# Performance work log

Measured on AMD Instinct MI355X. Metric: run time of the kernel, lower is better.

Reference implementation:

```python
import jax, jax.numpy as jnp
import numpy as np

EPS = 1e-8
VOX_WIDTH = 1.0
CURV_THRESH = 0.5


def _build_kernels():
    """Nine 3x3x3 central finite-difference stencils, pre-divided by vox_width / vox_width^2."""
    def zk():
        return np.zeros((3, 3, 3), np.float32)
    ks = {}
    # first derivatives (central difference), denominator vox_width
    for name, ax in (('ddx', 0), ('ddy', 1), ('ddz', 2)):
        k = zk(); i = [1, 1, 1]
        i[ax] = 0; k[tuple(i)] = -0.5
        i[ax] = 2; k[tuple(i)] = 0.5
        ks[name] = k / VOX_WIDTH
    # pure second derivatives, denominator vox_width^2
    for name, ax in (('d2dx2', 0), ('d2dy2', 1), ('d2dz2', 2)):
        k = zk(); i = [1, 1, 1]
        i[ax] = 0; k[tuple(i)] = 1.0
        i[ax] = 1; k[tuple(i)] = -2.0
        i[ax] = 2; k[tuple(i)] = 1.0
        ks[name] = k / VOX_WIDTH ** 2
    # mixed second derivatives, denominator vox_width^2
    for name, (a, b) in (('d2dxdy', (0, 1)), ('d2dxdz', (0, 2)), ('d2dydz', (1, 2))):
        k = zk()
        for sa, sb, v in ((0, 0, 0.25), (0, 2, -0.25), (2, 0, -0.25), (2, 2, 0.25)):
            i = [1, 1, 1]; i[a] = sa; i[b] = sb; k[tuple(i)] = v
        ks[name] = k / VOX_WIDTH ** 2
    order = ['ddx', 'ddy', 'ddz', 'd2dx2', 'd2dy2', 'd2dz2', 'd2dxdy', 'd2dxdz', 'd2dydz']
    return np.stack([ks[n] for n in order])[:, None]  # [9, 1, 3, 3, 3]


_KERNELS = jnp.asarray(_build_kernels())


def setup_inputs() -> dict:
    key = jax.random.key(0)
    phi = jax.random.normal(key, (2, 1, 192, 192, 192), dtype=jnp.float32)
    return {"phi": phi}


def reference(phi):
    # all nine stencils as one valid 3D conv: [N, 9, D-2, H-2, W-2]
    g = jax.lax.conv_general_dilated(
        phi, _KERNELS, window_strides=(1, 1, 1), padding='VALID',
        dimension_numbers=('NCDHW', 'OIDHW', 'NCDHW'))
    gx, gy, gz, hxx, hyy, hzz, hxy, hxz, hyz = (g[:, i:i + 1] for i in range(9))

    mag = jnp.sqrt(gx * gx + gy * gy + gz * gz + EPS)
    mag3 = mag ** 3

    # mean curvature: sum_{i!=j} g_i^2 H_jj - 2 sum_{i<j} g_i g_j H_ij, over |grad|^3
    cross = gx * gy * hxy + gx * gz * hxz + gy * gz * hyz
    mean_c = (gx * gx * (hyy + hzz) + gy * gy * (hxx + hzz) + gz * gz * (hxx + hyy)
              - 2.0 * cross) / (mag3 + EPS)

    # gaussian curvature: laplacian/|grad| - (g^T H g)/|grad|^3
    lap = (hxx + hyy + hzz) / (mag + EPS)
    quad = (gx * gx * hxx + gy * gy * hyy + gz * gz * hzz + 2.0 * cross) / (mag3 + EPS)
    gauss = lap - quad

    k1 = mean_c + jnp.sqrt(jnp.abs(mean_c ** 2 - gauss) + EPS)
    pen = jax.nn.relu((k1 / (CURV_THRESH + EPS)) ** 2 - 1.0)

    # zero crossings of phi over 3x3x3 neighborhoods (valid -> matches conv output shape)
    mn = jax.lax.reduce_window(phi, jnp.inf, jax.lax.min, (1, 1, 3, 3, 3), (1, 1, 1, 1, 1), 'VALID')
    mx = jax.lax.reduce_window(phi, -jnp.inf, jax.lax.max, (1, 1, 3, 3, 3), (1, 1, 1, 1, 1), 'VALID')
    phi_zero = jax.lax.stop_gradient((mn * mx < 0).astype(phi.dtype))

    return jnp.sum(phi_zero * pen) / (jnp.sum(phi_zero) + EPS)
```

## Files before the change

### kernel.cpp

```cpp
#include <hip/hip_runtime.h>


typedef float v2f __attribute__((ext_vector_type(2)));

constexpr int DIM  = 192;
constexpr int ODIM = 190;
constexpr int TX = 32, TY = 32, CZ = 10;
constexpr int NTX = 6, NTY = 6, NTZ = 19;
constexpr int PLANE = DIM * DIM;
constexpr int NBLOCKS = 2 * NTZ * NTY * NTX;

struct Slice {
    v2f   q[3][4];
    float mn[6], mx[6];
};

__global__ __launch_bounds__(256) void curv_main(const float* __restrict__ phi,
                                                 double* __restrict__ acc,
                                                 int use_partials) {
    int bx = blockIdx.x;
    const int tx = bx % NTX; bx /= NTX;
    const int ty = bx % NTY; bx /= NTY;
    const int tz = bx % NTZ; bx /= NTZ;
    const int n  = bx;

    const int xbase = tx * TX, ybase = ty * TY, zbase = tz * CZ;
    const int tid = threadIdx.x;
    const int row = tid >> 3;
    const int x0  = (tid & 7) * 4;
    const float* pn = phi + (long long)n * DIM * PLANE;

    const int c4 = xbase + x0;
    int c2t = c4 + 4; if (c2t > DIM - 2) c2t = DIM - 2;
    const int c2 = c2t;
    int yoff[3];
#pragma unroll
    for (int dy = 0; dy < 3; ++dy) {
        int iy = ybase + row + dy; if (iy > DIM - 1) iy = DIM - 1;
        yoff[dy] = iy * DIM;
    }

    float4 t4[3]; float2 t2[3];
    auto pref = [&](int g) {
        int gz = zbase + g; if (gz > DIM - 1) gz = DIM - 1;
        const float* base = pn + gz * PLANE;
#pragma unroll
        for (int dy = 0; dy < 3; ++dy) {
            t4[dy] = *(const float4*)(base + yoff[dy] + c4);
            t2[dy] = *(const float2*)(base + yoff[dy] + c2);
        }
    };

    auto unpack = [&](Slice& s) {
#pragma unroll
        for (int dy = 0; dy < 3; ++dy) {
            const float4 a = t4[dy]; const float2 b = t2[dy];
            s.q[dy][0] = (v2f){a.x, a.z};
            s.q[dy][1] = (v2f){a.y, a.w};
            s.q[dy][2] = (v2f){a.z, b.x};
            s.q[dy][3] = (v2f){a.w, b.y};
            if (dy == 0) {
                s.mn[0] = a.x; s.mn[1] = a.y; s.mn[2] = a.z;
                s.mn[3] = a.w; s.mn[4] = b.x; s.mn[5] = b.y;
                s.mx[0] = a.x; s.mx[1] = a.y; s.mx[2] = a.z;
                s.mx[3] = a.w; s.mx[4] = b.x; s.mx[5] = b.y;
            } else {
                s.mn[0] = fminf(s.mn[0], a.x); s.mx[0] = fmaxf(s.mx[0], a.x);
                s.mn[1] = fminf(s.mn[1], a.y); s.mx[1] = fmaxf(s.mx[1], a.y);
                s.mn[2] = fminf(s.mn[2], a.z); s.mx[2] = fmaxf(s.mx[2], a.z);
                s.mn[3] = fminf(s.mn[3], a.w); s.mx[3] = fmaxf(s.mx[3], a.w);
                s.mn[4] = fminf(s.mn[4], b.x); s.mx[4] = fmaxf(s.mx[4], b.x);
                s.mn[5] = fminf(s.mn[5], b.y); s.mx[5] = fmaxf(s.mx[5], b.y);
            }
        }
    };

    double sp = 0.0, sc = 0.0;
    const float EPSF = 1e-8f;
    const int oy = ybase + row;

    bool vmask[4];
#pragma unroll
    for (int j = 0; j < 4; ++j)
        vmask[j] = (oy < ODIM) && (xbase + x0 + j < ODIM);

    auto compute = [&](const Slice& s0, const Slice& s1, const Slice& s2) {
        float colmn[6], colmx[6];
#pragma unroll
        for (int c = 0; c < 6; ++c) {
            colmn[c] = fminf(fminf(s0.mn[c], s1.mn[c]), s2.mn[c]);
            colmx[c] = fmaxf(fmaxf(s0.mx[c], s1.mx[c]), s2.mx[c]);
        }

        float fsp = 0.0f, fsc = 0.0f;
#pragma unroll
        for (int p = 0; p < 2; ++p) {
            v2f gx = 0.5f * (s2.q[1][p + 1] - s0.q[1][p + 1]);
            v2f gy = 0.5f * (s1.q[2][p + 1] - s1.q[0][p + 1]);
            v2f gz = 0.5f * (s1.q[1][p + 2] - s1.q[1][p]);

            v2f c2v = 2.0f * s1.q[1][p + 1];
            v2f hxx = s0.q[1][p + 1] - c2v + s2.q[1][p + 1];
            v2f hyy = s1.q[0][p + 1] - c2v + s1.q[2][p + 1];
            v2f hzz = s1.q[1][p] - c2v + s1.q[1][p + 2];

            v2f hxy = 0.25f * (s0.q[0][p + 1] - s0.q[2][p + 1]
                             - s2.q[0][p + 1] + s2.q[2][p + 1]);
            v2f hxz = 0.25f * (s0.q[1][p] - s0.q[1][p + 2]
                             - s2.q[1][p] + s2.q[1][p + 2]);
            v2f hyz = 0.25f * (s1.q[0][p] - s1.q[0][p + 2]
                             - s1.q[2][p] + s1.q[2][p + 2]);

            v2f gx2 = gx * gx, gy2 = gy * gy, gz2 = gz * gz;
            v2f mag2 = gx2 + gy2 + gz2 + EPSF;

            v2f inv1 = (v2f){ __builtin_amdgcn_rsqf(mag2.x),
                              __builtin_amdgcn_rsqf(mag2.y) };
            v2f inv3 = inv1 * inv1 * inv1;

            v2f cross = gx * gy * hxy + gx * gz * hxz + gy * gz * hyz;

            v2f mean_c = (gx2 * (hyy + hzz) + gy2 * (hxx + hzz) +
                          gz2 * (hxx + hyy) - 2.0f * cross) * inv3;
            v2f lap   = (hxx + hyy + hzz) * inv1;
            v2f quad  = (gx2 * hxx + gy2 * hyy + gz2 * hzz + 2.0f * cross) * inv3;
            v2f gauss = lap - quad;

            v2f disc = mean_c * mean_c - gauss;
            v2f sq = (v2f){ sqrtf(fabsf(disc.x) + EPSF),
                            sqrtf(fabsf(disc.y) + EPSF) };
            v2f k1 = mean_c + sq;
            v2f t  = 2.0f * k1;
            v2f pen2 = t * t - 1.0f;

#pragma unroll
            for (int e = 0; e < 2; ++e) {
                const int j = p + 2 * e;
                float pen = fmaxf(e ? pen2.y : pen2.x, 0.0f);
                float mn = fminf(fminf(colmn[j], colmn[j + 1]), colmn[j + 2]);
                float mx = fmaxf(fmaxf(colmx[j], colmx[j + 1]), colmx[j + 2]);
                if (vmask[j] && (mn * mx < 0.0f)) {
                    fsp += pen;
                    fsc += 1.0f;
                }
            }
        }
        sp += (double)fsp;
        sc += (double)fsc;
    };

    Slice s0, s1, s2;

    pref(0); unpack(s0);
    pref(1); unpack(s1);
    pref(2);

    unpack(s2); pref(3);  compute(s0, s1, s2);
    unpack(s0); pref(4);  compute(s1, s2, s0);
    unpack(s1); pref(5);  compute(s2, s0, s1);
    unpack(s2); pref(6);  compute(s0, s1, s2);
    unpack(s0); pref(7);  compute(s1, s2, s0);
    unpack(s1); pref(8);  compute(s2, s0, s1);
    unpack(s2); pref(9);  compute(s0, s1, s2);
    unpack(s0); pref(10); compute(s1, s2, s0);
    unpack(s1); pref(11); compute(s2, s0, s1);
    unpack(s2);           compute(s0, s1, s2);

#pragma unroll
    for (int off = 32; off > 0; off >>= 1) {
        sp += __shfl_down(sp, off, 64);
        sc += __shfl_down(sc, off, 64);
    }

    __shared__ double lsp[4], lsc[4];
    const int wave = tid >> 6, lane = tid & 63;
    if (lane == 0) { lsp[wave] = sp; lsc[wave] = sc; }
    __syncthreads();
    if (tid == 0) {
        double tp = lsp[0] + lsp[1] + lsp[2] + lsp[3];
        double tc = lsc[0] + lsc[1] + lsc[2] + lsc[3];
        if (use_partials) {
            acc[2 * blockIdx.x]     = tp;
            acc[2 * blockIdx.x + 1] = tc;
        } else {
            atomicAdd(&acc[0], tp);
            atomicAdd(&acc[1], tc);
        }
    }
}

__global__ __launch_bounds__(256) void curv_reduce(const double* __restrict__ part,
                                                   int nblocks, int use_partials,
                                                   float* __restrict__ out) {
    double sp = 0.0, sc = 0.0;
    if (use_partials) {
        for (int i = threadIdx.x; i < nblocks; i += 256) {
            sp += part[2 * i];
            sc += part[2 * i + 1];
        }
    } else if (threadIdx.x == 0) {
        sp = part[0]; sc = part[1];
    }
#pragma unroll
    for (int off = 32; off > 0; off >>= 1) {
        sp += __shfl_down(sp, off, 64);
        sc += __shfl_down(sc, off, 64);
    }
    __shared__ double lsp[4], lsc[4];
    const int wave = threadIdx.x >> 6, lane = threadIdx.x & 63;
    if (lane == 0) { lsp[wave] = sp; lsc[wave] = sc; }
    __syncthreads();
    if (threadIdx.x == 0) {
        double tp = lsp[0] + lsp[1] + lsp[2] + lsp[3];
        double tc = lsc[0] + lsc[1] + lsc[2] + lsc[3];
        out[0] = (float)(tp / (tc + 1e-8));
    }
}

extern "C" void kernel_launch(void* const* d_in, const int* in_sizes, int n_in,
                              void* d_out, int out_size, void* d_ws, size_t ws_size,
                              hipStream_t stream) {
    const float* phi = (const float*)d_in[0];
    float* out = (float*)d_out;
    double* acc = (double*)d_ws;

    const int use_partials = (ws_size >= (size_t)(2 * NBLOCKS) * sizeof(double)) ? 1 : 0;
    if (!use_partials) {
        hipMemsetAsync(d_ws, 0, 2 * sizeof(double), stream);
    }

    curv_main<<<NBLOCKS, 256, 0, stream>>>(phi, acc, use_partials);
    curv_reduce<<<1, 256, 0, stream>>>(acc, NBLOCKS, use_partials, out);
}
```

Before: 109.2 us.

## Deepen z-chunk, precompute x-window min/max per slice, fold stencil scale factors

Doubles the z-chunk each block walks (19 planes instead of 10), halving the number of blocks and the halo planes reloaded per block. Per-slice min/max is now reduced across the 3-wide x window during unpack, so compute does fewer min/max operations. The 0.5 and 0.25 stencil scales are folded into the curvature formulas algebraically, with EPS scaled to match, and accumulation stays in float across the chunk instead of converting to double every step. Launch bounds now request occupancy 3, and the z clamp is dropped because the new chunking never reads past the last plane.

```diff
diff --git a/kernel.cpp b/kernel.cpp
--- a/kernel.cpp
+++ b/kernel.cpp
@@ -5,19 +5,19 @@
 
 constexpr int DIM  = 192;
 constexpr int ODIM = 190;
-constexpr int TX = 32, TY = 32, CZ = 10;
-constexpr int NTX = 6, NTY = 6, NTZ = 19;
+constexpr int TX = 32, TY = 32, CZ = 19;
+constexpr int NTX = 6, NTY = 6, NTZ = 10;
 constexpr int PLANE = DIM * DIM;
 constexpr int NBLOCKS = 2 * NTZ * NTY * NTX;
 
 struct Slice {
     v2f   q[3][4];
-    float mn[6], mx[6];
+    float xmn[4], xmx[4];
 };
 
-__global__ __launch_bounds__(256) void curv_main(const float* __restrict__ phi,
-                                                 double* __restrict__ acc,
-                                                 int use_partials) {
+__global__ __launch_bounds__(256, 3) void curv_main(const float* __restrict__ phi,
+                                                    double* __restrict__ acc,
+                                                    int use_partials) {
     int bx = blockIdx.x;
     const int tx = bx % NTX; bx /= NTX;
     const int ty = bx % NTY; bx /= NTY;
@@ -42,8 +42,7 @@
 
     float4 t4[3]; float2 t2[3];
     auto pref = [&](int g) {
-        int gz = zbase + g; if (gz > DIM - 1) gz = DIM - 1;
-        const float* base = pn + gz * PLANE;
+        const float* base = pn + (zbase + g) * PLANE;
 #pragma unroll
         for (int dy = 0; dy < 3; ++dy) {
             t4[dy] = *(const float4*)(base + yoff[dy] + c4);
@@ -52,6 +51,7 @@
     };
 
     auto unpack = [&](Slice& s) {
+        float mn6[6], mx6[6];
 #pragma unroll
         for (int dy = 0; dy < 3; ++dy) {
             const float4 a = t4[dy]; const float2 b = t2[dy];
@@ -60,23 +60,29 @@
             s.q[dy][2] = (v2f){a.z, b.x};
             s.q[dy][3] = (v2f){a.w, b.y};
             if (dy == 0) {
-                s.mn[0] = a.x; s.mn[1] = a.y; s.mn[2] = a.z;
-                s.mn[3] = a.w; s.mn[4] = b.x; s.mn[5] = b.y;
-                s.mx[0] = a.x; s.mx[1] = a.y; s.mx[2] = a.z;
-                s.mx[3] = a.w; s.mx[4] = b.x; s.mx[5] = b.y;
+                mn6[0] = a.x; mn6[1] = a.y; mn6[2] = a.z;
+                mn6[3] = a.w; mn6[4] = b.x; mn6[5] = b.y;
+                mx6[0] = a.x; mx6[1] = a.y; mx6[2] = a.z;
+                mx6[3] = a.w; mx6[4] = b.x; mx6[5] = b.y;
             } else {
-                s.mn[0] = fminf(s.mn[0], a.x); s.mx[0] = fmaxf(s.mx[0], a.x);
-                s.mn[1] = fminf(s.mn[1], a.y); s.mx[1] = fmaxf(s.mx[1], a.y);
-                s.mn[2] = fminf(s.mn[2], a.z); s.mx[2] = fmaxf(s.mx[2], a.z);
-                s.mn[3] = fminf(s.mn[3], a.w); s.mx[3] = fmaxf(s.mx[3], a.w);
-                s.mn[4] = fminf(s.mn[4], b.x); s.mx[4] = fmaxf(s.mx[4], b.x);
-                s.mn[5] = fminf(s.mn[5], b.y); s.mx[5] = fmaxf(s.mx[5], b.y);
+                mn6[0] = fminf(mn6[0], a.x); mx6[0] = fmaxf(mx6[0], a.x);
+                mn6[1] = fminf(mn6[1], a.y); mx6[1] = fmaxf(mx6[1], a.y);
+                mn6[2] = fminf(mn6[2], a.z); mx6[2] = fmaxf(mx6[2], a.z);
+                mn6[3] = fminf(mn6[3], a.w); mx6[3] = fmaxf(mx6[3], a.w);
+                mn6[4] = fminf(mn6[4], b.x); mx6[4] = fmaxf(mx6[4], b.x);
+                mn6[5] = fminf(mn6[5], b.y); mx6[5] = fmaxf(mx6[5], b.y);
             }
         }
+#pragma unroll
+        for (int j = 0; j < 4; ++j) {
+            s.xmn[j] = fminf(fminf(mn6[j], mn6[j + 1]), mn6[j + 2]);
+            s.xmx[j] = fmaxf(fmaxf(mx6[j], mx6[j + 1]), mx6[j + 2]);
+        }
     };
 
-    double sp = 0.0, sc = 0.0;
+    float fsp = 0.0f, fsc = 0.0f;
     const float EPSF = 1e-8f;
+    const float EPS4 = 4e-8f;
     const int oy = ybase + row;
 
     bool vmask[4];
@@ -85,45 +91,47 @@
         vmask[j] = (oy < ODIM) && (xbase + x0 + j < ODIM);
 
     auto compute = [&](const Slice& s0, const Slice& s1, const Slice& s2) {
-        float colmn[6], colmx[6];
-#pragma unroll
-        for (int c = 0; c < 6; ++c) {
-            colmn[c] = fminf(fminf(s0.mn[c], s1.mn[c]), s2.mn[c]);
-            colmx[c] = fmaxf(fmaxf(s0.mx[c], s1.mx[c]), s2.mx[c]);
-        }
-
-        float fsp = 0.0f, fsc = 0.0f;
+        float wmn[4], wmx[4];
+#pragma unroll
+        for (int j = 0; j < 4; ++j) {
+            wmn[j] = fminf(fminf(s0.xmn[j], s1.xmn[j]), s2.xmn[j]);
+            wmx[j] = fmaxf(fmaxf(s0.xmx[j], s1.xmx[j]), s2.xmx[j]);
+        }
+
 #pragma unroll
         for (int p = 0; p < 2; ++p) {
-            v2f gx = 0.5f * (s2.q[1][p + 1] - s0.q[1][p + 1]);
-            v2f gy = 0.5f * (s1.q[2][p + 1] - s1.q[0][p + 1]);
-            v2f gz = 0.5f * (s1.q[1][p + 2] - s1.q[1][p]);
+            v2f Gx = s2.q[1][p + 1] - s0.q[1][p + 1];
+            v2f Gy = s1.q[2][p + 1] - s1.q[0][p + 1];
+            v2f Gz = s1.q[1][p + 2] - s1.q[1][p];
 
             v2f c2v = 2.0f * s1.q[1][p + 1];
             v2f hxx = s0.q[1][p + 1] - c2v + s2.q[1][p + 1];
             v2f hyy = s1.q[0][p + 1] - c2v + s1.q[2][p + 1];
             v2f hzz = s1.q[1][p] - c2v + s1.q[1][p + 2];
 
-            v2f hxy = 0.25f * (s0.q[0][p + 1] - s0.q[2][p + 1]
-                             - s2.q[0][p + 1] + s2.q[2][p + 1]);
-            v2f hxz = 0.25f * (s0.q[1][p] - s0.q[1][p + 2]
-                             - s2.q[1][p] + s2.q[1][p + 2]);
-            v2f hyz = 0.25f * (s1.q[0][p] - s1.q[0][p + 2]
-                             - s1.q[2][p] + s1.q[2][p + 2]);
-
-            v2f gx2 = gx * gx, gy2 = gy * gy, gz2 = gz * gz;
-            v2f mag2 = gx2 + gy2 + gz2 + EPSF;
-
-            v2f inv1 = (v2f){ __builtin_amdgcn_rsqf(mag2.x),
-                              __builtin_amdgcn_rsqf(mag2.y) };
-            v2f inv3 = inv1 * inv1 * inv1;
-
-            v2f cross = gx * gy * hxy + gx * gz * hxz + gy * gz * hyz;
-
-            v2f mean_c = (gx2 * (hyy + hzz) + gy2 * (hxx + hzz) +
-                          gz2 * (hxx + hyy) - 2.0f * cross) * inv3;
-            v2f lap   = (hxx + hyy + hzz) * inv1;
-            v2f quad  = (gx2 * hxx + gy2 * hyy + gz2 * hzz + 2.0f * cross) * inv3;
+            v2f Mxy = s0.q[0][p + 1] - s0.q[2][p + 1]
+                    - s2.q[0][p + 1] + s2.q[2][p + 1];
+            v2f Mxz = s0.q[1][p] - s0.q[1][p + 2]
+                    - s2.q[1][p] + s2.q[1][p + 2];
+            v2f Myz = s1.q[0][p] - s1.q[0][p + 2]
+                    - s1.q[2][p] + s1.q[2][p + 2];
+
+            v2f Gx2 = Gx * Gx, Gy2 = Gy * Gy, Gz2 = Gz * Gz;
+            v2f mag2G = Gx2 + Gy2 + Gz2 + EPS4;
+
+            v2f r = (v2f){ __builtin_amdgcn_rsqf(mag2G.x),
+                           __builtin_amdgcn_rsqf(mag2G.y) };
+            v2f r3 = r * r * r;
+            v2f twor3 = r3 + r3;
+
+            v2f crossG = Gx * Gy * Mxy + Gx * Gz * Mxz + Gy * Gz * Myz;
+
+            v2f num1 = Gx2 * (hyy + hzz) + Gy2 * (hxx + hzz) +
+                       Gz2 * (hxx + hyy) - 0.5f * crossG;
+            v2f mean_c = num1 * twor3;
+            v2f lap   = (hxx + hyy + hzz) * (r + r);
+            v2f num2  = Gx2 * hxx + Gy2 * hyy + Gz2 * hzz + 0.5f * crossG;
+            v2f quad  = num2 * twor3;
             v2f gauss = lap - quad;
 
             v2f disc = mean_c * mean_c - gauss;
@@ -137,16 +145,12 @@
             for (int e = 0; e < 2; ++e) {
                 const int j = p + 2 * e;
                 float pen = fmaxf(e ? pen2.y : pen2.x, 0.0f);
-                float mn = fminf(fminf(colmn[j], colmn[j + 1]), colmn[j + 2]);
-                float mx = fmaxf(fmaxf(colmx[j], colmx[j + 1]), colmx[j + 2]);
-                if (vmask[j] && (mn * mx < 0.0f)) {
+                if (vmask[j] && (wmn[j] * wmx[j] < 0.0f)) {
                     fsp += pen;
                     fsc += 1.0f;
                 }
             }
         }
-        sp += (double)fsp;
-        sc += (double)fsc;
     };
 
     Slice s0, s1, s2;
@@ -164,8 +168,18 @@
     unpack(s2); pref(9);  compute(s0, s1, s2);
     unpack(s0); pref(10); compute(s1, s2, s0);
     unpack(s1); pref(11); compute(s2, s0, s1);
+    unpack(s2); pref(12); compute(s0, s1, s2);
+    unpack(s0); pref(13); compute(s1, s2, s0);
+    unpack(s1); pref(14); compute(s2, s0, s1);
+    unpack(s2); pref(15); compute(s0, s1, s2);
+    unpack(s0); pref(16); compute(s1, s2, s0);
+    unpack(s1); pref(17); compute(s2, s0, s1);
+    unpack(s2); pref(18); compute(s0, s1, s2);
+    unpack(s0); pref(19); compute(s1, s2, s0);
+    unpack(s1); pref(20); compute(s2, s0, s1);
     unpack(s2);           compute(s0, s1, s2);
 
+    double sp = (double)fsp, sc = (double)fsc;
 #pragma unroll
     for (int off = 32; off > 0; off >>= 1) {
         sp += __shfl_down(sp, off, 64);
```

Result: faster. 105.7 us (-3.3%).
